# Performance work log

Hardware: AMD Instinct MI355X
Metric: run time of the kernel (lower is better)

The kernel has to match this reference:

```python
import jax, jax.numpy as jnp
import numpy as np

HIDDEN = 4096
N_HEADS = 32
N_KV_HEADS = 2
HEAD_DIM = 128          # hidden // n_heads
ROT_DIM = HEAD_DIM // 2  # partial rotary (ChatGLM style)
ROPE_THETA = 10000.0
Q_SIZE = N_HEADS * HEAD_DIM
KV_SIZE = N_KV_HEADS * HEAD_DIM
SCALE = HEAD_DIM ** -0.5
T = 2048


def setup_inputs() -> dict:
    key = jax.random.key(0)
    k1, k2, k3, k4 = jax.random.split(key, 4)
    hidden_states = jax.random.normal(k1, (T, HIDDEN), dtype=jnp.float32)
    positions = jnp.arange(T, dtype=jnp.int64) if jax.config.jax_enable_x64 else jnp.arange(T, dtype=jnp.int32)
    w_qkv = jax.random.normal(k2, (Q_SIZE + 2 * KV_SIZE, HIDDEN), dtype=jnp.float32) * 0.02
    b_qkv = jax.random.normal(k3, (Q_SIZE + 2 * KV_SIZE,), dtype=jnp.float32) * 0.02
    w_dense = jax.random.normal(k4, (HIDDEN, Q_SIZE), dtype=jnp.float32) * 0.02
    return {"hidden_states": hidden_states, "positions": positions,
            "w_qkv": w_qkv, "b_qkv": b_qkv, "w_dense": w_dense}


def _apply_rope(x, positions):
    # x: [T, H, HEAD_DIM]; interleaved (is_neox_style=False) partial rotary on first ROT_DIM dims
    half = ROT_DIM // 2
    inv_freq = 1.0 / (ROPE_THETA ** (jnp.arange(0, half, dtype=jnp.float32) * 2.0 / ROT_DIM))
    freqs = positions.astype(jnp.float32)[:, None] * inv_freq[None, :]   # [T, half]
    cos = jnp.cos(freqs)[:, None, :]  # [T, 1, half]
    sin = jnp.sin(freqs)[:, None, :]
    x_rot = x[..., :ROT_DIM]
    x_pass = x[..., ROT_DIM:]
    x1 = x_rot[..., 0::2]
    x2 = x_rot[..., 1::2]
    o1 = x1 * cos - x2 * sin
    o2 = x2 * cos + x1 * sin
    rot = jnp.stack([o1, o2], axis=-1).reshape(x_rot.shape)  # re-interleave
    return jnp.concatenate([rot, x_pass], axis=-1)


def reference(hidden_states, positions, w_qkv, b_qkv, w_dense):
    # QKV projection (bias from add_qkv_bias=True)
    qkv = hidden_states @ w_qkv.T + b_qkv                     # [T, 4608]
    q = qkv[:, :Q_SIZE].reshape(T, N_HEADS, HEAD_DIM)
    k = qkv[:, Q_SIZE:Q_SIZE + KV_SIZE].reshape(T, N_KV_HEADS, HEAD_DIM)
    v = qkv[:, Q_SIZE + KV_SIZE:].reshape(T, N_KV_HEADS, HEAD_DIM)

    q = _apply_rope(q, positions)
    k = _apply_rope(k, positions)

    # GQA: expand 2 kv heads -> 32 q heads (each kv head serves 16 q heads)
    rep = N_HEADS // N_KV_HEADS
    k = jnp.repeat(k, rep, axis=1)                            # [T, 32, 128]
    v = jnp.repeat(v, rep, axis=1)

    # Causal scaled dot-product attention
    scores = jnp.einsum('thd,shd->hts', q, k) * SCALE         # [H, T, T]
    causal = positions[:, None] >= positions[None, :]          # [T, T]
    scores = jnp.where(causal[None, :, :], scores, jnp.finfo(scores.dtype).min)
    probs = jax.nn.softmax(scores, axis=-1)
    attn = jnp.einsum('hts,shd->thd', probs, v).reshape(T, Q_SIZE)

    # Output projection (no bias: add_bias_linear=False)
    return attn @ w_dense.T
```

## Files before the change

kernel.cpp:

```cpp
#include <hip/hip_runtime.h>
#include <cstdint>
#include <math.h>

typedef __bf16 bf16;
typedef __bf16 bf16x8 __attribute__((ext_vector_type(8)));
typedef __bf16 bf16x4 __attribute__((ext_vector_type(4)));
typedef float f32x4 __attribute__((ext_vector_type(4)));

#define T_SEQ 2048
#define HID   4096
#define NQH   32
#define NKVH  2
#define HD    128
#define NQKV  4608
#define ATT_SCALE 0.08838834764831845f

#define VMCNT(n) asm volatile("s_waitcnt vmcnt(" #n ")" ::: "memory")

__device__ __forceinline__ void load_lds16(const void* g, void* l) {
    auto gp = (const __attribute__((address_space(1))) unsigned int*)(uintptr_t)g;
    auto lp = (__attribute__((address_space(3))) unsigned int*)(unsigned int)(uintptr_t)l;
    __builtin_amdgcn_global_load_lds(gp, lp, 16, 0, 0);
}

__device__ __forceinline__ f32x4 mfma16(bf16x8 a, bf16x8 b, f32x4 c) {
    return __builtin_amdgcn_mfma_f32_16x16x32_bf16(a, b, c, 0, 0, 0);
}

__global__ void cvt_f32_bf16_kernel(const float* __restrict__ x, bf16* __restrict__ y) {
    size_t i = ((size_t)blockIdx.x * 256 + threadIdx.x) * 8;
    float4 a = *(const float4*)(x + i);
    float4 b = *(const float4*)(x + i + 4);
    bf16x8 o;
    o[0] = (bf16)a.x; o[1] = (bf16)a.y; o[2] = (bf16)a.z; o[3] = (bf16)a.w;
    o[4] = (bf16)b.x; o[5] = (bf16)b.y; o[6] = (bf16)b.z; o[7] = (bf16)b.w;
    *(bf16x8*)(y + i) = o;
}

template <int OUT_BF16, int HAS_BIAS>
__global__ __launch_bounds__(256) void gemm_bt(const bf16* __restrict__ A,
                                               const bf16* __restrict__ B,
                                               const float* __restrict__ bias,
                                               void* __restrict__ Cout,
                                               int M, int N, int K) {
    __shared__ __align__(16) char sA[16384];
    __shared__ __align__(16) char sB[16384];
    const int tid = threadIdx.x;
    const int wid = tid >> 6, l = tid & 63, l4 = l >> 4, l16 = l & 15;
    const int wm = wid >> 1, wn = wid & 1;
    const int bm = blockIdx.x * 128, bn = blockIdx.y * 128;

    f32x4 acc[4][4] = {};

    for (int k0 = 0; k0 < K; k0 += 64) {
        __syncthreads();
#pragma unroll
        for (int c4 = 0; c4 < 4; ++c4) {
            int ch = c4 * 256 + tid;
            int row = ch >> 3, cch = ch & 7;
            int scc = cch ^ (row & 7);
            load_lds16(A + (size_t)(bm + row) * K + k0 + scc * 8,
                       sA + c4 * 4096 + wid * 1024);
        }
#pragma unroll
        for (int c4 = 0; c4 < 4; ++c4) {
            int ch = c4 * 256 + tid;
            int row = ch >> 3, cch = ch & 7;
            int scc = cch ^ (row & 7);
            load_lds16(B + (size_t)(bn + row) * K + k0 + scc * 8,
                       sB + c4 * 4096 + wid * 1024);
        }
        __syncthreads();
#pragma unroll
        for (int ks = 0; ks < 2; ++ks) {
            bf16x8 af[4], bfr[4];
#pragma unroll
            for (int mi = 0; mi < 4; ++mi) {
                int row = wm * 64 + mi * 16 + l16;
                af[mi] = *(const bf16x8*)(sA + row * 128 + ((ks * 64 + l4 * 16) ^ ((row & 7) << 4)));
            }
#pragma unroll
            for (int ni = 0; ni < 4; ++ni) {
                int row = wn * 64 + ni * 16 + l16;
                bfr[ni] = *(const bf16x8*)(sB + row * 128 + ((ks * 64 + l4 * 16) ^ ((row & 7) << 4)));
            }
#pragma unroll
            for (int mi = 0; mi < 4; ++mi)
#pragma unroll
                for (int ni = 0; ni < 4; ++ni)
                    acc[mi][ni] = mfma16(af[mi], bfr[ni], acc[mi][ni]);
        }
    }

#pragma unroll
    for (int mi = 0; mi < 4; ++mi)
#pragma unroll
        for (int ni = 0; ni < 4; ++ni) {
            const int col = bn + wn * 64 + ni * 16 + l16;
            float bv = HAS_BIAS ? bias[col] : 0.0f;
#pragma unroll
            for (int r = 0; r < 4; ++r) {
                const int row = bm + wm * 64 + mi * 16 + l4 * 4 + r;
                float val = acc[mi][ni][r] + bv;
                if (OUT_BF16)
                    ((bf16*)Cout)[(size_t)row * N + col] = (bf16)val;
                else
                    ((float*)Cout)[(size_t)row * N + col] = val;
            }
        }
}

__global__ void rope_qk_kernel(const bf16* __restrict__ qkv,
                               bf16* __restrict__ qheads, bf16* __restrict__ kheads) {
    const int t = blockIdx.x;
    const int g = blockIdx.y;
    const int sub = threadIdx.x >> 6;
    const int l = threadIdx.x & 63;
    const bf16* src;
    bf16* dst;
    if (g < 8) {
        int hh = g * 4 + sub;
        src = qkv + (size_t)t * NQKV + hh * HD;
        dst = qheads + ((size_t)hh * T_SEQ + t) * HD;
    } else {
        if (sub >= 2) return;
        src = qkv + (size_t)t * NQKV + HID + sub * HD;
        dst = kheads + ((size_t)sub * T_SEQ + t) * HD;
    }
    if (l < 32) {
        const int i = l;
        float x1 = (float)src[2 * i], x2 = (float)src[2 * i + 1];
        float fr = (float)t * exp2f((float)i * (-13.287712379549449f / 32.0f));
        float sn = sinf(fr), cs = cosf(fr);
        dst[2 * i] = (bf16)(x1 * cs - x2 * sn);
        dst[2 * i + 1] = (bf16)(x2 * cs + x1 * sn);
    } else {
        const int j = l - 32;
        dst[64 + 2 * j] = src[64 + 2 * j];
        dst[64 + 2 * j + 1] = src[64 + 2 * j + 1];
    }
}

__global__ void v_trans_kernel(const bf16* __restrict__ qkv, bf16* __restrict__ vt) {
    const int t0 = blockIdx.x * 64;
    const int kvh = blockIdx.y;
    const int tid = threadIdx.x;
#pragma unroll
    for (int it = 0; it < 4; ++it) {
        int ch = it * 256 + tid;
        int d = ch >> 3, tc = ch & 7;
        int t = t0 + tc * 8;
        const bf16* src = qkv + (size_t)t * NQKV + 4352 + kvh * HD + d;
        bf16x8 v;
#pragma unroll
        for (int i = 0; i < 8; ++i) v[i] = src[(size_t)i * NQKV];
        *(bf16x8*)(vt + ((size_t)kvh * HD + d) * T_SEQ + t) = v;
    }
}

__global__ __launch_bounds__(256, 1) void attn_fwd_kernel(const bf16* __restrict__ qh,
                                                          const bf16* __restrict__ kh,
                                                          const bf16* __restrict__ vt,
                                                          bf16* __restrict__ attnb) {
    __shared__ __align__(16) char sK[2][16384];
    __shared__ __align__(16) char sV[16384];
    __shared__ __align__(16) char sP[4][4096];
    const int tid = threadIdx.x;
    const int wid = tid >> 6, l = tid & 63, l4 = l >> 4, l16 = l & 15;
    const int b = blockIdx.x;
    const int qb = 15 - (b >> 5);
    const int h = b & 31, kvh = h >> 4;
    const int qbase = qb * 128 + wid * 32;

    auto stageK = [&](int buf, int kt) {
#pragma unroll
        for (int c4 = 0; c4 < 4; ++c4) {
            int ch = c4 * 256 + tid;
            int row = ch >> 4, cc = ch & 15;
            load_lds16(kh + ((size_t)kvh * T_SEQ + kt * 64 + row) * HD + (cc ^ (row & 7)) * 8,
                       sK[buf] + c4 * 4096 + wid * 1024);
        }
    };
    auto stageV = [&](int kt) {
#pragma unroll
        for (int c4 = 0; c4 < 4; ++c4) {
            int ch = c4 * 256 + tid;
            int row = ch >> 3, cc = ch & 7;
            load_lds16(vt + ((size_t)kvh * HD + row) * T_SEQ + kt * 64 + (cc ^ (row & 7)) * 8,
                       sV + c4 * 4096 + wid * 1024);
        }
    };

    bf16x8 qf[2][4];
#pragma unroll
    for (int rg = 0; rg < 2; ++rg) {
        const bf16* qp = qh + ((size_t)h * T_SEQ + qbase + rg * 16 + l16) * HD + l4 * 8;
#pragma unroll
        for (int f = 0; f < 4; ++f) qf[rg][f] = *(const bf16x8*)(qp + f * 32);
    }
    VMCNT(0);
    stageK(0, 0);

    f32x4 o[2][8] = {};
    float mr[2][4], lr[2][4];
#pragma unroll
    for (int rg = 0; rg < 2; ++rg)
#pragma unroll
        for (int r = 0; r < 4; ++r) { mr[rg][r] = -INFINITY; lr[rg][r] = 0.f; }

    const int nt = 2 * qb + 2;
    int cur = 0;
    for (int kt = 0; kt < nt; ++kt) {
        const bool havenext = (kt + 1 < nt);
        __builtin_amdgcn_s_barrier();
        __builtin_amdgcn_sched_barrier(0);
        stageV(kt);
        if (havenext) stageK(cur ^ 1, kt + 1);
        if (havenext) { VMCNT(16); } else { VMCNT(8); }
        __builtin_amdgcn_s_barrier();
        __builtin_amdgcn_sched_barrier(0);

        const bool active = (kt * 64) <= (qbase + 31);
        if (active) {
            f32x4 s[2][4] = {};
#pragma unroll
            for (int ct = 0; ct < 4; ++ct)
#pragma unroll
                for (int ks = 0; ks < 4; ++ks) {
                    int row = ct * 16 + l16;
                    bf16x8 kf = *(const bf16x8*)(sK[cur] + row * 256 + ((ks * 64 + l4 * 16) ^ ((row & 7) << 4)));
                    s[0][ct] = mfma16(qf[0][ks], kf, s[0][ct]);
                    s[1][ct] = mfma16(qf[1][ks], kf, s[1][ct]);
                }

            const bool diag = (kt * 64 + 63 > qbase);
            float sv[2][4][4];
#pragma unroll
            for (int rg = 0; rg < 2; ++rg)
#pragma unroll
                for (int ct = 0; ct < 4; ++ct)
#pragma unroll
                    for (int r = 0; r < 4; ++r) {
                        float x = s[rg][ct][r] * ATT_SCALE;
                        if (diag && (kt * 64 + ct * 16 + l16) > (qbase + rg * 16 + l4 * 4 + r)) x = -INFINITY;
                        sv[rg][ct][r] = x;
                    }

            float pmx[2][4];
            bool ok = true;
#pragma unroll
            for (int rg = 0; rg < 2; ++rg)
#pragma unroll
                for (int r = 0; r < 4; ++r) {
                    pmx[rg][r] = fmaxf(fmaxf(sv[rg][0][r], sv[rg][1][r]), fmaxf(sv[rg][2][r], sv[rg][3][r]));
                    ok = ok && (pmx[rg][r] <= mr[rg][r] + 8.0f);
                }
            if (!__all(ok)) {
#pragma unroll
                for (int rg = 0; rg < 2; ++rg)
#pragma unroll
                    for (int r = 0; r < 4; ++r) {
                        float mx = pmx[rg][r];
                        mx = fmaxf(mx, __shfl_xor(mx, 1));
                        mx = fmaxf(mx, __shfl_xor(mx, 2));
                        mx = fmaxf(mx, __shfl_xor(mx, 4));
                        mx = fmaxf(mx, __shfl_xor(mx, 8));
                        if (mx > mr[rg][r]) {
                            float al = __expf(mr[rg][r] - mx);
                            mr[rg][r] = mx;
                            lr[rg][r] *= al;
#pragma unroll
                            for (int n2 = 0; n2 < 8; ++n2) o[rg][n2][r] *= al;
                        }
                    }
            }
#pragma unroll
            for (int rg = 0; rg < 2; ++rg)
#pragma unroll
                for (int r = 0; r < 4; ++r) {
                    float ps = 0.f;
                    const int prow = rg * 16 + l4 * 4 + r;
#pragma unroll
                    for (int ct = 0; ct < 4; ++ct) {
                        float p = __expf(sv[rg][ct][r] - mr[rg][r]);
                        ps += p;
                        *(bf16*)(sP[wid] + prow * 128 + (((ct * 16 + l16) * 2) ^ ((prow & 7) << 4))) = (bf16)p;
                    }
                    lr[rg][r] += ps;
                }
        }

        if (havenext) { VMCNT(8); } else { VMCNT(0); }
        __builtin_amdgcn_s_barrier();
        __builtin_amdgcn_sched_barrier(0);

        if (active) {
#pragma unroll
            for (int ks = 0; ks < 2; ++ks) {
                bf16x8 pa0 = *(const bf16x8*)(sP[wid] + l16 * 128 + ((ks * 64 + l4 * 16) ^ ((l16 & 7) << 4)));
                bf16x8 pa1 = *(const bf16x8*)(sP[wid] + (16 + l16) * 128 + ((ks * 64 + l4 * 16) ^ ((l16 & 7) << 4)));
#pragma unroll
                for (int n2 = 0; n2 < 8; ++n2) {
                    int vrow = n2 * 16 + l16;
                    bf16x8 vf = *(const bf16x8*)(sV + vrow * 128 + ((ks * 64 + l4 * 16) ^ ((vrow & 7) << 4)));
                    o[0][n2] = mfma16(pa0, vf, o[0][n2]);
                    o[1][n2] = mfma16(pa1, vf, o[1][n2]);
                }
            }
        }
        cur ^= 1;
    }

    float inv[2][4];
#pragma unroll
    for (int rg = 0; rg < 2; ++rg)
#pragma unroll
        for (int r = 0; r < 4; ++r) {
            float s2 = lr[rg][r];
            s2 += __shfl_xor(s2, 1);
            s2 += __shfl_xor(s2, 2);
            s2 += __shfl_xor(s2, 4);
            s2 += __shfl_xor(s2, 8);
            inv[rg][r] = 1.0f / s2;
        }
#pragma unroll
    for (int rg = 0; rg < 2; ++rg)
#pragma unroll
        for (int n2 = 0; n2 < 8; ++n2)
#pragma unroll
            for (int r = 0; r < 4; ++r) {
                int row = qb * 128 + wid * 32 + rg * 16 + l4 * 4 + r;
                int col = h * HD + n2 * 16 + l16;
                attnb[(size_t)row * HID + col] = (bf16)(o[rg][n2][r] * inv[rg][r]);
            }
}

extern "C" void kernel_launch(void* const* d_in, const int* in_sizes, int n_in,
                              void* d_out, int out_size, void* d_ws, size_t ws_size,
                              hipStream_t stream) {
    const float* hs = (const float*)d_in[0];
    const float* wqkv = (const float*)d_in[2];
    const float* bqkv = (const float*)d_in[3];
    const float* wdense = (const float*)d_in[4];
    float* out = (float*)d_out;

    char* ws = (char*)d_ws;
    bf16* wqkvb   = (bf16*)(ws + 0);
    bf16* hb      = (bf16*)(ws + 37748736);
    bf16* qkvb    = (bf16*)(ws + 54525952);
    bf16* qhp     = (bf16*)(ws + 0);
    bf16* khp     = (bf16*)(ws + 16777216);
    bf16* vtp     = (bf16*)(ws + 17825792);
    bf16* wdenseb = (bf16*)(ws + 18874368);
    bf16* attnb   = (bf16*)(ws + 54525952);
    (void)in_sizes; (void)n_in; (void)out_size; (void)ws_size;

    cvt_f32_bf16_kernel<<<(T_SEQ * HID) / 2048, 256, 0, stream>>>(hs, hb);
    cvt_f32_bf16_kernel<<<(NQKV * HID) / 2048, 256, 0, stream>>>(wqkv, wqkvb);

    dim3 g1(T_SEQ / 128, NQKV / 128);
    gemm_bt<1, 1><<<g1, 256, 0, stream>>>(hb, wqkvb, bqkv, (void*)qkvb, T_SEQ, NQKV, HID);

    cvt_f32_bf16_kernel<<<(HID * HID) / 2048, 256, 0, stream>>>(wdense, wdenseb);

    rope_qk_kernel<<<dim3(T_SEQ, 9), 256, 0, stream>>>(qkvb, qhp, khp);
    v_trans_kernel<<<dim3(T_SEQ / 64, NKVH), 256, 0, stream>>>(qkvb, vtp);

    attn_fwd_kernel<<<512, 256, 0, stream>>>(qhp, khp, vtp, attnb);

    dim3 g2(T_SEQ / 128, HID / 128);
    gemm_bt<0, 0><<<g2, 256, 0, stream>>>(attnb, wdenseb, nullptr, (void*)out, T_SEQ, HID, HID);
}
```

Measured before the change: 341.1 us.

## Switch GEMM to 32x32x16 MFMA with two waves per 128x128 tile

Rewrites the bf16 GEMM used for the QKV and dense projections so each block runs 2 waves instead of 4. Each wave computes a 128x64 slice using 32x32x16 MFMA instructions with 16-float accumulators, in place of 16x16x32 tiles. Each wave now loads 4 A fragments and 2 B fragments per k-step, so fewer LDS reads are needed per MFMA. In exchange, per-wave register use rises and each block has half as many waves to hide global-to-LDS load latency.

```diff
diff --git a/kernel.cpp b/kernel.cpp
--- a/kernel.cpp
+++ b/kernel.cpp
@@ -6,6 +6,7 @@
 typedef __bf16 bf16x8 __attribute__((ext_vector_type(8)));
 typedef __bf16 bf16x4 __attribute__((ext_vector_type(4)));
 typedef float f32x4 __attribute__((ext_vector_type(4)));
+typedef float f32x16 __attribute__((ext_vector_type(16)));
 
 #define T_SEQ 2048
 #define HID   4096
@@ -38,7 +39,7 @@
 }
 
 template <int OUT_BF16, int HAS_BIAS>
-__global__ __launch_bounds__(256) void gemm_bt(const bf16* __restrict__ A,
+__global__ __launch_bounds__(128) void gemm_bt(const bf16* __restrict__ A,
                                                const bf16* __restrict__ B,
                                                const float* __restrict__ bias,
                                                void* __restrict__ Cout,
@@ -46,62 +47,61 @@
     __shared__ __align__(16) char sA[16384];
     __shared__ __align__(16) char sB[16384];
     const int tid = threadIdx.x;
-    const int wid = tid >> 6, l = tid & 63, l4 = l >> 4, l16 = l & 15;
-    const int wm = wid >> 1, wn = wid & 1;
+    const int wid = tid >> 6, l = tid & 63;
+    const int l32 = l & 31, lh = l >> 5;
     const int bm = blockIdx.x * 128, bn = blockIdx.y * 128;
 
-    f32x4 acc[4][4] = {};
+    f32x16 acc[4][2] = {};
 
     for (int k0 = 0; k0 < K; k0 += 64) {
         __syncthreads();
 #pragma unroll
-        for (int c4 = 0; c4 < 4; ++c4) {
-            int ch = c4 * 256 + tid;
-            int row = ch >> 3, cch = ch & 7;
-            int scc = cch ^ (row & 7);
-            load_lds16(A + (size_t)(bm + row) * K + k0 + scc * 8,
-                       sA + c4 * 4096 + wid * 1024);
-        }
-#pragma unroll
-        for (int c4 = 0; c4 < 4; ++c4) {
-            int ch = c4 * 256 + tid;
-            int row = ch >> 3, cch = ch & 7;
-            int scc = cch ^ (row & 7);
-            load_lds16(B + (size_t)(bn + row) * K + k0 + scc * 8,
-                       sB + c4 * 4096 + wid * 1024);
+        for (int c8 = 0; c8 < 8; ++c8) {
+            int ch = c8 * 128 + tid;
+            int row = ch >> 3, cc = ch & 7;
+            load_lds16(A + (size_t)(bm + row) * K + k0 + (cc ^ (row & 7)) * 8,
+                       sA + c8 * 2048 + wid * 1024);
+        }
+#pragma unroll
+        for (int c8 = 0; c8 < 8; ++c8) {
+            int ch = c8 * 128 + tid;
+            int row = ch >> 3, cc = ch & 7;
+            load_lds16(B + (size_t)(bn + row) * K + k0 + (cc ^ (row & 7)) * 8,
+                       sB + c8 * 2048 + wid * 1024);
         }
         __syncthreads();
 #pragma unroll
-        for (int ks = 0; ks < 2; ++ks) {
-            bf16x8 af[4], bfr[4];
+        for (int ks = 0; ks < 4; ++ks) {
+            const int kcol = ks * 32 + lh * 16;
+            bf16x8 af[4], bfr[2];
 #pragma unroll
             for (int mi = 0; mi < 4; ++mi) {
-                int row = wm * 64 + mi * 16 + l16;
-                af[mi] = *(const bf16x8*)(sA + row * 128 + ((ks * 64 + l4 * 16) ^ ((row & 7) << 4)));
-            }
-#pragma unroll
-            for (int ni = 0; ni < 4; ++ni) {
-                int row = wn * 64 + ni * 16 + l16;
-                bfr[ni] = *(const bf16x8*)(sB + row * 128 + ((ks * 64 + l4 * 16) ^ ((row & 7) << 4)));
+                int row = mi * 32 + l32;
+                af[mi] = *(const bf16x8*)(sA + row * 128 + (kcol ^ ((row & 7) << 4)));
+            }
+#pragma unroll
+            for (int ni = 0; ni < 2; ++ni) {
+                int row = wid * 64 + ni * 32 + l32;
+                bfr[ni] = *(const bf16x8*)(sB + row * 128 + (kcol ^ ((row & 7) << 4)));
             }
 #pragma unroll
             for (int mi = 0; mi < 4; ++mi)
 #pragma unroll
-                for (int ni = 0; ni < 4; ++ni)
-                    acc[mi][ni] = mfma16(af[mi], bfr[ni], acc[mi][ni]);
+                for (int ni = 0; ni < 2; ++ni)
+                    acc[mi][ni] = __builtin_amdgcn_mfma_f32_32x32x16_bf16(af[mi], bfr[ni], acc[mi][ni], 0, 0, 0);
         }
     }
 
 #pragma unroll
     for (int mi = 0; mi < 4; ++mi)
 #pragma unroll
-        for (int ni = 0; ni < 4; ++ni) {
-            const int col = bn + wn * 64 + ni * 16 + l16;
+        for (int ni = 0; ni < 2; ++ni) {
+            const int col = bn + wid * 64 + ni * 32 + l32;
             float bv = HAS_BIAS ? bias[col] : 0.0f;
 #pragma unroll
-            for (int r = 0; r < 4; ++r) {
-                const int row = bm + wm * 64 + mi * 16 + l4 * 4 + r;
-                float val = acc[mi][ni][r] + bv;
+            for (int reg = 0; reg < 16; ++reg) {
+                const int row = bm + mi * 32 + (reg & 3) + 8 * (reg >> 2) + 4 * lh;
+                float val = acc[mi][ni][reg] + bv;
                 if (OUT_BF16)
                     ((bf16*)Cout)[(size_t)row * N + col] = (bf16)val;
                 else
@@ -359,7 +359,7 @@
     cvt_f32_bf16_kernel<<<(NQKV * HID) / 2048, 256, 0, stream>>>(wqkv, wqkvb);
 
     dim3 g1(T_SEQ / 128, NQKV / 128);
-    gemm_bt<1, 1><<<g1, 256, 0, stream>>>(hb, wqkvb, bqkv, (void*)qkvb, T_SEQ, NQKV, HID);
+    gemm_bt<1, 1><<<g1, 128, 0, stream>>>(hb, wqkvb, bqkv, (void*)qkvb, T_SEQ, NQKV, HID);
 
     cvt_f32_bf16_kernel<<<(HID * HID) / 2048, 256, 0, stream>>>(wdense, wdenseb);
 
@@ -369,5 +369,5 @@
     attn_fwd_kernel<<<512, 256, 0, stream>>>(qhp, khp, vtp, attnb);
 
     dim3 g2(T_SEQ / 128, HID / 128);
-    gemm_bt<0, 0><<<g2, 256, 0, stream>>>(attnb, wdenseb, nullptr, (void*)out, T_SEQ, HID, HID);
-}
+    gemm_bt<0, 0><<<g2, 128, 0, stream>>>(attnb, wdenseb, nullptr, (void*)out, T_SEQ, HID, HID);
+}
```

Result: slower. 407.0 us (+19.3%).
